# Kernel optimization log

Hardware: AMD Instinct MI355X
Metric: run time of the kernel (lower is better)

The kernel has to match this reference:

```python
import jax, jax.numpy as jnp
import numpy as np

N = 16384
IN_DIM = 128
OUT_DIM = 128
NUM_TYPES = 8


def setup_inputs() -> dict:
    key = jax.random.key(0)
    k1, k2, k3, k4 = jax.random.split(key, 4)
    x = jax.random.normal(k1, (N, IN_DIM), dtype=jnp.float32)
    node_types = jax.random.randint(k2, (N,), 0, NUM_TYPES, dtype=jnp.int32)
    adjacency = jax.random.uniform(k3, (N, N), dtype=jnp.float32)
    weight = jax.random.normal(k4, (NUM_TYPES, OUT_DIM, IN_DIM), dtype=jnp.float32)
    return {"x": x, "node_types": node_types, "adjacency": adjacency, "weight": weight}


def reference(x, node_types, adjacency, weight):
    # agg = A @ x : (N, in_dim)
    agg = jnp.matmul(adjacency, x)
    # Per-type projection: compute agg @ W[t].T for all types, then select
    # by node type. (N, T, out) intermediate is small (N*T*out floats).
    per_type = jnp.einsum("nd,tod->nto", agg, weight)  # (N, T, out)
    out = jnp.take_along_axis(per_type, node_types[:, None, None].astype(jnp.int32), axis=1)
    return out[:, 0, :]  # (N, out)
```

## Files before the change

kernel.cpp:

```cpp
#include <hip/hip_runtime.h>
#include <stdint.h>


#define N_NODES 16384
#define DIM     128
#define NTYPES  8
#define BM      64
#define BK      128
#define NT_K    (N_NODES / BK)

typedef float  f32x4  __attribute__((ext_vector_type(4)));
typedef __bf16 bf16x4 __attribute__((ext_vector_type(4)));
typedef __bf16 bf16x8 __attribute__((ext_vector_type(8)));

__device__ __attribute__((aligned(16))) unsigned short g_xT[DIM * N_NODES];
__device__ __attribute__((aligned(16))) unsigned short g_Wb[NTYPES * DIM * DIM];

__device__ __forceinline__ unsigned int f2b(float f) {
    unsigned int u = __float_as_uint(f);
    u += 0x7FFFu + ((u >> 16) & 1u);
    return u >> 16;
}
#define BF_LO(u) __uint_as_float((unsigned int)(u) << 16)
#define BF_HI(u) __uint_as_float((unsigned int)(u) & 0xFFFF0000u)

__device__ __forceinline__ bf16x4 cvt4(const f32x4 v) {
    bf16x4 r;
    r[0] = (__bf16)v[0]; r[1] = (__bf16)v[1]; r[2] = (__bf16)v[2]; r[3] = (__bf16)v[3];
    return r;
}


__global__ void prep_all(const float* __restrict__ x, const float* __restrict__ w) {
    const int tid = threadIdx.x;
    if (blockIdx.x < 64) {
        int n = blockIdx.x * 256 + tid;
        const float* row = x + (size_t)n * DIM;
#pragma unroll
        for (int d0 = 0; d0 < DIM; d0 += 4) {
            float4 v = *(const float4*)(row + d0);
            g_xT[(d0 + 0) * N_NODES + n] = (unsigned short)f2b(v.x);
            g_xT[(d0 + 1) * N_NODES + n] = (unsigned short)f2b(v.y);
            g_xT[(d0 + 2) * N_NODES + n] = (unsigned short)f2b(v.z);
            g_xT[(d0 + 3) * N_NODES + n] = (unsigned short)f2b(v.w);
        }
    } else {
        int base = ((blockIdx.x - 64) * 256 + tid) * 16;
#pragma unroll
        for (int j = 0; j < 4; ++j) {
            float4 v = *(const float4*)(w + base + j * 4);
            ushort4 o;
            o.x = (unsigned short)f2b(v.x); o.y = (unsigned short)f2b(v.y);
            o.z = (unsigned short)f2b(v.z); o.w = (unsigned short)f2b(v.w);
            *(ushort4*)(g_Wb + base + j * 4) = o;
        }
    }
}


#define AB_BYTES 16384
#define XB_BYTES 32768

#define GLOAD16(g, l) __builtin_amdgcn_global_load_lds(                         \
    (const __attribute__((address_space(1))) unsigned int*)(g),                 \
    (__attribute__((address_space(3))) unsigned int*)(l), 16, 0, 0)

#define ALOADI(reg, ptr, off) \
    asm volatile("global_load_dwordx4 %0, %1, off offset:" #off : "=v"(reg) : "v"(ptr))

#define ISSUE_AL4() do {                                                   \
    ALOADI(p0, pA0, 0); ALOADI(q0, pA0, 512); ALOADI(r0, pA0, 1024); ALOADI(s0, pA0, 1536); \
    ALOADI(p1, pA1, 0); ALOADI(q1, pA1, 512); ALOADI(r1, pA1, 1024); ALOADI(s1, pA1, 1536); \
    ALOADI(p2, pA2, 0); ALOADI(q2, pA2, 512); ALOADI(r2, pA2, 1024); ALOADI(s2, pA2, 1536); \
    ALOADI(p3, pA3, 0); ALOADI(q3, pA3, 512); ALOADI(r3, pA3, 1024); ALOADI(s3, pA3, 1536); \
    pA0 += 512; pA1 += 512; pA2 += 512; pA3 += 512;                        \
} while (0)

#define ISSUE_XD(Xb) do {                        \
    GLOAD16(gX0, (Xb) + 0 * 8192 + wq);          \
    GLOAD16(gX1, (Xb) + 1 * 8192 + wq);          \
    GLOAD16(gX2, (Xb) + 2 * 8192 + wq);          \
    GLOAD16(gX3, (Xb) + 3 * 8192 + wq);          \
    gX0 += BK; gX1 += BK; gX2 += BK; gX3 += BK;  \
} while (0)

#define STOREA(As, R0, R1, R2, R3) do {          \
    *(bf16x4*)((As) + aw0) = cvt4(R0);           \
    *(bf16x4*)((As) + aw1) = cvt4(R1);           \
    *(bf16x4*)((As) + aw2) = cvt4(R2);           \
    *(bf16x4*)((As) + aw3) = cvt4(R3);           \
} while (0)

#define KS(Ab, Xb, off) do {                                                    \
    bf16x8 a0_ = *(const bf16x8*)((Ab) + arA0 + (off));                         \
    bf16x8 a1_ = *(const bf16x8*)((Ab) + arA1 + (off));                         \
    bf16x8 b0_ = *(const bf16x8*)((Xb) + xB0 + (off));                          \
    bf16x8 b1_ = *(const bf16x8*)((Xb) + xB1 + (off));                          \
    acc00 = __builtin_amdgcn_mfma_f32_16x16x32_bf16(a0_, b0_, acc00, 0, 0, 0);  \
    acc01 = __builtin_amdgcn_mfma_f32_16x16x32_bf16(a0_, b1_, acc01, 0, 0, 0);  \
    acc10 = __builtin_amdgcn_mfma_f32_16x16x32_bf16(a1_, b0_, acc10, 0, 0, 0);  \
    acc11 = __builtin_amdgcn_mfma_f32_16x16x32_bf16(a1_, b1_, acc11, 0, 0, 0);  \
} while (0)

#define COMPUTE(Ab, Xb) do {      \
    KS(Ab, Xb, off0);             \
    KS(Ab, Xb, off1);             \
    KS(Ab, Xb, off2);             \
    KS(Ab, Xb, off3);             \
} while (0)

#define WAITV(N) do {                                        \
    asm volatile("s_waitcnt vmcnt(" #N ")" ::: "memory");    \
    __builtin_amdgcn_sched_barrier(0);                       \
} while (0)

#define TOP(VM) do {                                                            \
    asm volatile("s_waitcnt vmcnt(" #VM ") lgkmcnt(0)\n\ts_barrier" ::: "memory"); \
    __builtin_amdgcn_sched_barrier(0);                                          \
} while (0)

#define PH_A0(Xc, Xi) do { TOP(4);  COMPUTE(Ab0, Xc); STOREA(Ab1, q0,q1,q2,q3); ISSUE_XD(Xi); } while (0)
#define PH_A1(Xc, Xi) do { TOP(4);  COMPUTE(Ab1, Xc); STOREA(Ab0, r0,r1,r2,r3); ISSUE_XD(Xi); } while (0)
#define PH_A2(Xc, Xi) do { TOP(4);  COMPUTE(Ab0, Xc); STOREA(Ab1, s0,s1,s2,s3); ISSUE_AL4(); ISSUE_XD(Xi); } while (0)
#define PH_A3(Xc, Xi) do { TOP(20); COMPUTE(Ab1, Xc); WAITV(7); STOREA(Ab0, p0,p1,p2,p3); ISSUE_XD(Xi); } while (0)

__global__ __launch_bounds__(512, 1) void gconv_main(
    const float* __restrict__ adj,
    const int* __restrict__ types,
    float* __restrict__ out)
{
    __shared__ __align__(16) unsigned char lds[3 * XB_BYTES + 2 * AB_BYTES];
    unsigned char* X0 = lds;
    unsigned char* X1 = lds + XB_BYTES;
    unsigned char* X2 = lds + 2 * XB_BYTES;
    unsigned char* Ab0 = lds + 3 * XB_BYTES;
    unsigned char* Ab1 = Ab0 + AB_BYTES;

    const int tid  = threadIdx.x;
    const int w    = tid >> 6;
    const int l    = tid & 63;
    const int m0   = blockIdx.x * BM;

    const int mrow = (w & 1) * 32;
    const int ncol = (w >> 1) * 32;
    const int h    = l >> 4;

    f32x4 acc00 = {}, acc01 = {}, acc10 = {}, acc11 = {};

    const int rj0 = w * 8 + 0 + (l >> 5);
    const int rj1 = w * 8 + 2 + (l >> 5);
    const int rj2 = w * 8 + 4 + (l >> 5);
    const int rj3 = w * 8 + 6 + (l >> 5);
    const float* pA0 = adj + (size_t)(m0 + rj0) * N_NODES + (l & 31) * 4;
    const float* pA1 = adj + (size_t)(m0 + rj1) * N_NODES + (l & 31) * 4;
    const float* pA2 = adj + (size_t)(m0 + rj2) * N_NODES + (l & 31) * 4;
    const float* pA3 = adj + (size_t)(m0 + rj3) * N_NODES + (l & 31) * 4;
    const int g_  = l & 31;
    const int aw0 = rj0 * 256 + ((((g_ >> 1) ^ (rj0 & 7))) << 4) + ((g_ & 1) << 3);
    const int aw1 = rj1 * 256 + ((((g_ >> 1) ^ (rj1 & 7))) << 4) + ((g_ & 1) << 3);
    const int aw2 = rj2 * 256 + ((((g_ >> 1) ^ (rj2 & 7))) << 4) + ((g_ & 1) << 3);
    const int aw3 = rj3 * 256 + ((((g_ >> 1) ^ (rj3 & 7))) << 4) + ((g_ & 1) << 3);

    const int xdw = 4 * w + (l >> 4);
    const unsigned short* gX0 = g_xT + (size_t)( 0 + xdw) * N_NODES + (((l & 15) ^ (xdw & 7)) << 3);
    const unsigned short* gX1 = g_xT + (size_t)(32 + xdw) * N_NODES + (((l & 15) ^ (xdw & 7)) << 3);
    const unsigned short* gX2 = g_xT + (size_t)(64 + xdw) * N_NODES + (((l & 15) ^ (xdw & 7)) << 3);
    const unsigned short* gX3 = g_xT + (size_t)(96 + xdw) * N_NODES + (((l & 15) ^ (xdw & 7)) << 3);
    const int wq = w << 10;

    const int arA0 = (mrow +  0 + (l & 15)) * 256;
    const int arA1 = (mrow + 16 + (l & 15)) * 256;
    const int xB0  = (ncol +  0 + (l & 15)) * 256;
    const int xB1  = (ncol + 16 + (l & 15)) * 256;
    const int off0 = (( 0 + h) ^ (l & 7)) << 4;
    const int off1 = (( 4 + h) ^ (l & 7)) << 4;
    const int off2 = (( 8 + h) ^ (l & 7)) << 4;
    const int off3 = ((12 + h) ^ (l & 7)) << 4;

    f32x4 p0, p1, p2, p3, q0, q1, q2, q3,
          r0, r1, r2, r3, s0, s1, s2, s3;

    ISSUE_AL4();
    ISSUE_XD(X0);
    ISSUE_XD(X1);
    WAITV(8);
    STOREA(Ab0, p0, p1, p2, p3);

    for (int i = 0; i < 10; ++i) {
        PH_A0(X0, X2); PH_A1(X1, X0); PH_A2(X2, X1); PH_A3(X0, X2);
        PH_A0(X1, X0); PH_A1(X2, X1); PH_A2(X0, X2); PH_A3(X1, X0);
        PH_A0(X2, X1); PH_A1(X0, X2); PH_A2(X1, X0); PH_A3(X2, X1);
    }
    PH_A0(X0, X2); PH_A1(X1, X0); PH_A2(X2, X1); PH_A3(X0, X2);
    TOP(4);
    COMPUTE(Ab0, X1);
    STOREA(Ab1, q0, q1, q2, q3);
    ISSUE_XD(X0);
    TOP(4);
    COMPUTE(Ab1, X2);
    STOREA(Ab0, r0, r1, r2, r3);
    ISSUE_XD(X1);
    TOP(4);
    COMPUTE(Ab0, X0);
    STOREA(Ab1, s0, s1, s2, s3);
    TOP(0);
    COMPUTE(Ab1, X1);
    __syncthreads();

    float* agg = (float*)lds;
#pragma unroll
    for (int rr = 0; rr < 4; ++rr) {
        const int e0 = (mrow +  0 + h * 4 + rr) * 132 + ncol + (l & 15);
        const int e1 = (mrow + 16 + h * 4 + rr) * 132 + ncol + (l & 15);
        agg[e0 +  0] = acc00[rr];
        agg[e0 + 16] = acc01[rr];
        agg[e1 +  0] = acc10[rr];
        agg[e1 + 16] = acc11[rr];
    }
    __syncthreads();

    const int rbase = w * 8;
    for (int rr = 0; rr < 8; ++rr) {
        const int rw = rbase + rr;
        const int nn = m0 + rw;
        const int ty = types[nn];
        const unsigned short* Wt = g_Wb + ty * (DIM * DIM);
        const int o0 = l * 2;
        const float* aggRow = agg + rw * 132;
        float t0 = 0.f, t1 = 0.f;
#pragma unroll
        for (int d0 = 0; d0 < DIM; d0 += 8) {
            float4 ga = *(const float4*)(aggRow + d0);
            float4 gb = *(const float4*)(aggRow + d0 + 4);
            uint4 wa = *(const uint4*)(Wt + o0 * DIM + d0);
            uint4 wb = *(const uint4*)(Wt + (o0 + 1) * DIM + d0);
            t0 += ga.x * BF_LO(wa.x) + ga.y * BF_HI(wa.x) + ga.z * BF_LO(wa.y) + ga.w * BF_HI(wa.y);
            t0 += gb.x * BF_LO(wa.z) + gb.y * BF_HI(wa.z) + gb.z * BF_LO(wa.w) + gb.w * BF_HI(wa.w);
            t1 += ga.x * BF_LO(wb.x) + ga.y * BF_HI(wb.x) + ga.z * BF_LO(wb.y) + ga.w * BF_HI(wb.y);
            t1 += gb.x * BF_LO(wb.z) + gb.y * BF_HI(wb.z) + gb.z * BF_LO(wb.w) + gb.w * BF_HI(wb.w);
        }
        float2 res; res.x = t0; res.y = t1;
        *(float2*)(out + (size_t)nn * DIM + o0) = res;
    }
}


extern "C" void kernel_launch(void* const* d_in, const int* in_sizes, int n_in,
                              void* d_out, int out_size, void* d_ws, size_t ws_size,
                              hipStream_t stream) {
    const float* x     = (const float*)d_in[0];
    const int*   types = (const int*)d_in[1];
    const float* adj   = (const float*)d_in[2];
    const float* wt    = (const float*)d_in[3];
    float* out = (float*)d_out;

    hipLaunchKernelGGL(prep_all, dim3(96), dim3(256), 0, stream, x, wt);
    hipLaunchKernelGGL(gconv_main, dim3(N_NODES / BM), dim3(512), 0, stream, adj, types, out);
}
```

Baseline: 285.8 us.

## Double workgroup to 1024 threads with 16 waves splitting the 64x128 tile

Raises the workgroup from 8 to 16 waves. Each wave now computes a 16x32 output sub-tile with two accumulators instead of 32x32 with four, and does half the adjacency and x-tile loads per phase. The vmcnt wait counts and the epilogue row mapping are adjusted to match. The goal is more waves in flight on each CU to hide the latency of streaming the fp32 adjacency from HBM. The cost is more barrier participants and less MFMA work per LDS read per wave.

```diff
diff --git a/kernel.cpp b/kernel.cpp
--- a/kernel.cpp
+++ b/kernel.cpp
@@ -68,38 +68,31 @@
 #define ALOADI(reg, ptr, off) \
     asm volatile("global_load_dwordx4 %0, %1, off offset:" #off : "=v"(reg) : "v"(ptr))
 
-#define ISSUE_AL4() do {                                                   \
-    ALOADI(p0, pA0, 0); ALOADI(q0, pA0, 512); ALOADI(r0, pA0, 1024); ALOADI(s0, pA0, 1536); \
-    ALOADI(p1, pA1, 0); ALOADI(q1, pA1, 512); ALOADI(r1, pA1, 1024); ALOADI(s1, pA1, 1536); \
-    ALOADI(p2, pA2, 0); ALOADI(q2, pA2, 512); ALOADI(r2, pA2, 1024); ALOADI(s2, pA2, 1536); \
-    ALOADI(p3, pA3, 0); ALOADI(q3, pA3, 512); ALOADI(r3, pA3, 1024); ALOADI(s3, pA3, 1536); \
-    pA0 += 512; pA1 += 512; pA2 += 512; pA3 += 512;                        \
+#define ISSUE_AL8() do {                          \
+    ALOADI(pa, pA,    0); ALOADI(pb, pA,  256);   \
+    ALOADI(qa, pA,  512); ALOADI(qb, pA,  768);   \
+    ALOADI(ra, pA, 1024); ALOADI(rb, pA, 1280);   \
+    ALOADI(sa, pA, 1536); ALOADI(sb, pA, 1792);   \
+    pA += 512;                                    \
 } while (0)
 
 #define ISSUE_XD(Xb) do {                        \
-    GLOAD16(gX0, (Xb) + 0 * 8192 + wq);          \
-    GLOAD16(gX1, (Xb) + 1 * 8192 + wq);          \
-    GLOAD16(gX2, (Xb) + 2 * 8192 + wq);          \
-    GLOAD16(gX3, (Xb) + 3 * 8192 + wq);          \
-    gX0 += BK; gX1 += BK; gX2 += BK; gX3 += BK;  \
-} while (0)
-
-#define STOREA(As, R0, R1, R2, R3) do {          \
-    *(bf16x4*)((As) + aw0) = cvt4(R0);           \
-    *(bf16x4*)((As) + aw1) = cvt4(R1);           \
-    *(bf16x4*)((As) + aw2) = cvt4(R2);           \
-    *(bf16x4*)((As) + aw3) = cvt4(R3);           \
+    GLOAD16(gX0, (Xb) + wq);                     \
+    GLOAD16(gX1, (Xb) + 16384 + wq);             \
+    gX0 += BK; gX1 += BK;                        \
+} while (0)
+
+#define STOREA(As, lo, hi) do {                  \
+    *(bf16x4*)((As) + awLo) = cvt4(lo);          \
+    *(bf16x4*)((As) + awHi) = cvt4(hi);          \
 } while (0)
 
 #define KS(Ab, Xb, off) do {                                                    \
-    bf16x8 a0_ = *(const bf16x8*)((Ab) + arA0 + (off));                         \
-    bf16x8 a1_ = *(const bf16x8*)((Ab) + arA1 + (off));                         \
+    bf16x8 a_  = *(const bf16x8*)((Ab) + arA + (off));                          \
     bf16x8 b0_ = *(const bf16x8*)((Xb) + xB0 + (off));                          \
     bf16x8 b1_ = *(const bf16x8*)((Xb) + xB1 + (off));                          \
-    acc00 = __builtin_amdgcn_mfma_f32_16x16x32_bf16(a0_, b0_, acc00, 0, 0, 0);  \
-    acc01 = __builtin_amdgcn_mfma_f32_16x16x32_bf16(a0_, b1_, acc01, 0, 0, 0);  \
-    acc10 = __builtin_amdgcn_mfma_f32_16x16x32_bf16(a1_, b0_, acc10, 0, 0, 0);  \
-    acc11 = __builtin_amdgcn_mfma_f32_16x16x32_bf16(a1_, b1_, acc11, 0, 0, 0);  \
+    acc00 = __builtin_amdgcn_mfma_f32_16x16x32_bf16(a_, b0_, acc00, 0, 0, 0);   \
+    acc01 = __builtin_amdgcn_mfma_f32_16x16x32_bf16(a_, b1_, acc01, 0, 0, 0);   \
 } while (0)
 
 #define COMPUTE(Ab, Xb) do {      \
@@ -119,12 +112,12 @@
     __builtin_amdgcn_sched_barrier(0);                                          \
 } while (0)
 
-#define PH_A0(Xc, Xi) do { TOP(4);  COMPUTE(Ab0, Xc); STOREA(Ab1, q0,q1,q2,q3); ISSUE_XD(Xi); } while (0)
-#define PH_A1(Xc, Xi) do { TOP(4);  COMPUTE(Ab1, Xc); STOREA(Ab0, r0,r1,r2,r3); ISSUE_XD(Xi); } while (0)
-#define PH_A2(Xc, Xi) do { TOP(4);  COMPUTE(Ab0, Xc); STOREA(Ab1, s0,s1,s2,s3); ISSUE_AL4(); ISSUE_XD(Xi); } while (0)
-#define PH_A3(Xc, Xi) do { TOP(20); COMPUTE(Ab1, Xc); WAITV(7); STOREA(Ab0, p0,p1,p2,p3); ISSUE_XD(Xi); } while (0)
-
-__global__ __launch_bounds__(512, 1) void gconv_main(
+#define PH_A0(Xc, Xi) do { TOP(2);  COMPUTE(Ab0, Xc); STOREA(Ab1, qa, qb); ISSUE_XD(Xi); } while (0)
+#define PH_A1(Xc, Xi) do { TOP(2);  COMPUTE(Ab1, Xc); STOREA(Ab0, ra, rb); ISSUE_XD(Xi); } while (0)
+#define PH_A2(Xc, Xi) do { TOP(2);  COMPUTE(Ab0, Xc); STOREA(Ab1, sa, sb); ISSUE_AL8(); ISSUE_XD(Xi); } while (0)
+#define PH_A3(Xc, Xi) do { TOP(10); COMPUTE(Ab1, Xc); WAITV(8); STOREA(Ab0, pa, pb); ISSUE_XD(Xi); } while (0)
+
+__global__ __launch_bounds__(1024, 1) void gconv_main(
     const float* __restrict__ adj,
     const int* __restrict__ types,
     float* __restrict__ out)
@@ -141,50 +134,39 @@
     const int l    = tid & 63;
     const int m0   = blockIdx.x * BM;
 
-    const int mrow = (w & 1) * 32;
-    const int ncol = (w >> 1) * 32;
+    const int mrow = (w & 3) * 16;
+    const int ncol = (w >> 2) * 32;
     const int h    = l >> 4;
 
-    f32x4 acc00 = {}, acc01 = {}, acc10 = {}, acc11 = {};
-
-    const int rj0 = w * 8 + 0 + (l >> 5);
-    const int rj1 = w * 8 + 2 + (l >> 5);
-    const int rj2 = w * 8 + 4 + (l >> 5);
-    const int rj3 = w * 8 + 6 + (l >> 5);
-    const float* pA0 = adj + (size_t)(m0 + rj0) * N_NODES + (l & 31) * 4;
-    const float* pA1 = adj + (size_t)(m0 + rj1) * N_NODES + (l & 31) * 4;
-    const float* pA2 = adj + (size_t)(m0 + rj2) * N_NODES + (l & 31) * 4;
-    const float* pA3 = adj + (size_t)(m0 + rj3) * N_NODES + (l & 31) * 4;
-    const int g_  = l & 31;
-    const int aw0 = rj0 * 256 + ((((g_ >> 1) ^ (rj0 & 7))) << 4) + ((g_ & 1) << 3);
-    const int aw1 = rj1 * 256 + ((((g_ >> 1) ^ (rj1 & 7))) << 4) + ((g_ & 1) << 3);
-    const int aw2 = rj2 * 256 + ((((g_ >> 1) ^ (rj2 & 7))) << 4) + ((g_ & 1) << 3);
-    const int aw3 = rj3 * 256 + ((((g_ >> 1) ^ (rj3 & 7))) << 4) + ((g_ & 1) << 3);
-
-    const int xdw = 4 * w + (l >> 4);
-    const unsigned short* gX0 = g_xT + (size_t)( 0 + xdw) * N_NODES + (((l & 15) ^ (xdw & 7)) << 3);
-    const unsigned short* gX1 = g_xT + (size_t)(32 + xdw) * N_NODES + (((l & 15) ^ (xdw & 7)) << 3);
-    const unsigned short* gX2 = g_xT + (size_t)(64 + xdw) * N_NODES + (((l & 15) ^ (xdw & 7)) << 3);
-    const unsigned short* gX3 = g_xT + (size_t)(96 + xdw) * N_NODES + (((l & 15) ^ (xdw & 7)) << 3);
+    f32x4 acc00 = {}, acc01 = {};
+
+    const int arow = w * 4 + (l >> 4);
+    const float* pA = adj + (size_t)(m0 + arow) * N_NODES + (l & 15) * 4;
+    const int gl  = (l & 15) >> 1;
+    const int sub = ((l & 15) & 1) << 3;
+    const int awLo = arow * 256 + (((gl)     ^ (arow & 7)) << 4) + sub;
+    const int awHi = arow * 256 + (((8 + gl) ^ (arow & 7)) << 4) + sub;
+
+    const int xd0 = w * 4 + (l >> 4);
+    const unsigned short* gX0 = g_xT + (size_t)xd0 * N_NODES + (((l & 15) ^ (xd0 & 7)) << 3);
+    const unsigned short* gX1 = g_xT + (size_t)(64 + xd0) * N_NODES + (((l & 15) ^ (xd0 & 7)) << 3);
     const int wq = w << 10;
 
-    const int arA0 = (mrow +  0 + (l & 15)) * 256;
-    const int arA1 = (mrow + 16 + (l & 15)) * 256;
-    const int xB0  = (ncol +  0 + (l & 15)) * 256;
-    const int xB1  = (ncol + 16 + (l & 15)) * 256;
+    const int arA = (mrow + (l & 15)) * 256;
+    const int xB0 = (ncol +  0 + (l & 15)) * 256;
+    const int xB1 = (ncol + 16 + (l & 15)) * 256;
     const int off0 = (( 0 + h) ^ (l & 7)) << 4;
     const int off1 = (( 4 + h) ^ (l & 7)) << 4;
     const int off2 = (( 8 + h) ^ (l & 7)) << 4;
     const int off3 = ((12 + h) ^ (l & 7)) << 4;
 
-    f32x4 p0, p1, p2, p3, q0, q1, q2, q3,
-          r0, r1, r2, r3, s0, s1, s2, s3;
-
-    ISSUE_AL4();
+    f32x4 pa, pb, qa, qb, ra, rb, sa, sb;
+
+    ISSUE_AL8();
     ISSUE_XD(X0);
     ISSUE_XD(X1);
-    WAITV(8);
-    STOREA(Ab0, p0, p1, p2, p3);
+    WAITV(4);
+    STOREA(Ab0, pa, pb);
 
     for (int i = 0; i < 10; ++i) {
         PH_A0(X0, X2); PH_A1(X1, X0); PH_A2(X2, X1); PH_A3(X0, X2);
@@ -192,17 +174,17 @@
         PH_A0(X2, X1); PH_A1(X0, X2); PH_A2(X1, X0); PH_A3(X2, X1);
     }
     PH_A0(X0, X2); PH_A1(X1, X0); PH_A2(X2, X1); PH_A3(X0, X2);
-    TOP(4);
+    TOP(2);
     COMPUTE(Ab0, X1);
-    STOREA(Ab1, q0, q1, q2, q3);
+    STOREA(Ab1, qa, qb);
     ISSUE_XD(X0);
-    TOP(4);
+    TOP(2);
     COMPUTE(Ab1, X2);
-    STOREA(Ab0, r0, r1, r2, r3);
+    STOREA(Ab0, ra, rb);
     ISSUE_XD(X1);
-    TOP(4);
+    TOP(2);
     COMPUTE(Ab0, X0);
-    STOREA(Ab1, s0, s1, s2, s3);
+    STOREA(Ab1, sa, sb);
     TOP(0);
     COMPUTE(Ab1, X1);
     __syncthreads();
@@ -210,17 +192,14 @@
     float* agg = (float*)lds;
 #pragma unroll
     for (int rr = 0; rr < 4; ++rr) {
-        const int e0 = (mrow +  0 + h * 4 + rr) * 132 + ncol + (l & 15);
-        const int e1 = (mrow + 16 + h * 4 + rr) * 132 + ncol + (l & 15);
+        const int e0 = (mrow + h * 4 + rr) * 132 + ncol + (l & 15);
         agg[e0 +  0] = acc00[rr];
         agg[e0 + 16] = acc01[rr];
-        agg[e1 +  0] = acc10[rr];
-        agg[e1 + 16] = acc11[rr];
     }
     __syncthreads();
 
-    const int rbase = w * 8;
-    for (int rr = 0; rr < 8; ++rr) {
+    const int rbase = w * 4;
+    for (int rr = 0; rr < 4; ++rr) {
         const int rw = rbase + rr;
         const int nn = m0 + rw;
         const int ty = types[nn];
@@ -255,5 +234,5 @@
     float* out = (float*)d_out;
 
     hipLaunchKernelGGL(prep_all, dim3(96), dim3(256), 0, stream, x, wt);
-    hipLaunchKernelGGL(gconv_main, dim3(N_NODES / BM), dim3(512), 0, stream, adj, types, out);
-}
+    hipLaunchKernelGGL(gconv_main, dim3(N_NODES / BM), dim3(1024), 0, stream, adj, types, out);
+}
```

After: 286.0 us. Within noise of the previous version (+0.1%).
